# Performance work log

Hardware: AMD Instinct MI355X
Metric: run time of the kernel (lower is better)

Reference implementation:

```python
import jax, jax.numpy as jnp
import numpy as np

E, K = 8, 2              # n_routed_experts, num_experts_per_tok
H, I = 2048, 1408        # hidden_size, moe_intermediate_size
IS = 2 * I               # shared experts intermediate (n_shared_experts * I)
B, S = 2, 512


def setup_inputs() -> dict:
    key = jax.random.key(0)
    ks = jax.random.split(key, 8)
    w = 0.02
    return {
        "hidden_states": jax.random.normal(ks[0], (B, S, H), jnp.float32),
        "router_w": jax.random.normal(ks[1], (E, H), jnp.float32) * w,
        "w_gate": jax.random.normal(ks[2], (E, I, H), jnp.float32) * w,
        "w_up": jax.random.normal(ks[3], (E, I, H), jnp.float32) * w,
        "w_down": jax.random.normal(ks[4], (E, H, I), jnp.float32) * w,
        "sw_gate": jax.random.normal(ks[5], (IS, H), jnp.float32) * w,
        "sw_up": jax.random.normal(ks[6], (IS, H), jnp.float32) * w,
        "sw_down": jax.random.normal(ks[7], (H, IS), jnp.float32) * w,
    }


def reference(hidden_states, router_w, w_gate, w_up, w_down, sw_gate, sw_up, sw_down):
    b, s, h = hidden_states.shape
    x = hidden_states.reshape(-1, h)                      # [T, H]
    t = x.shape[0]

    # Router: F.linear(x, gate_weight) -> softmax (fp32) -> topk (sorted)
    router_logits = x @ router_w.T                        # [T, E]
    scores = jax.nn.softmax(router_logits.astype(jnp.float32), axis=-1)
    routing_weights, selected = jax.lax.top_k(scores, K)  # [T, K]
    routing_weights = routing_weights / (routing_weights.sum(-1, keepdims=True) + 1e-6)
    routing_weights = routing_weights.astype(x.dtype)

    # Combine weights: [T, E], zero where expert not selected (exact gather/scatter math)
    cw = jnp.zeros((t, E), x.dtype).at[jnp.arange(t)[:, None], selected].add(routing_weights)

    # Per-expert SwiGLU FFN, batched over experts (grouped GEMM form)
    g = jnp.einsum('td,eid->eti', x, w_gate)              # [E, T, I]
    u = jnp.einsum('td,eid->eti', x, w_up)                # [E, T, I]
    y = jnp.einsum('eti,edi->etd', jax.nn.silu(g) * u, w_down)  # [E, T, H]
    moe_out = jnp.einsum('etd,te->td', y, cw)             # weighted combine -> [T, H]

    # Shared experts SwiGLU over all tokens
    shared = (jax.nn.silu(x @ sw_gate.T) * (x @ sw_up.T)) @ sw_down.T  # [T, H]

    final = (moe_out + shared).reshape(b, s, h)
    return final, router_logits
```

## Files before the change

kernel.cpp:

```cpp
#include <hip/hip_runtime.h>
#include <hip/hip_bf16.h>
#include <math.h>

#define T_TOK 1024
#define HDIM  2048
#define NEXP  8
#define IDIM  1408
#define ISH   2816
#define ROW_CAP 3072
#define ROWS_ALL 4096
#define MOE_TILES 24
#define NT_TOT 32

typedef __attribute__((ext_vector_type(8))) short bf16x8;
typedef __attribute__((ext_vector_type(4))) float f32x4;

static __device__ __forceinline__ unsigned short f2bf(float f) {
  __hip_bfloat16 h = __float2bfloat16(f);
  return __builtin_bit_cast(unsigned short, h);
}

__global__ __launch_bounds__(256) void router_kernel(
    const float* __restrict__ x, const float* __restrict__ rw,
    float* __restrict__ logits_out, int* __restrict__ selk, float* __restrict__ cwk)
{
  int t = blockIdx.x;
  int tid = threadIdx.x;
  float part[NEXP];
  const float* xr = x + (size_t)t * HDIM + tid * 8;
  float4 xa = *reinterpret_cast<const float4*>(xr);
  float4 xb = *reinterpret_cast<const float4*>(xr + 4);
  for (int e = 0; e < NEXP; ++e) {
    const float* wp = rw + (size_t)e * HDIM + tid * 8;
    float4 wa = *reinterpret_cast<const float4*>(wp);
    float4 wb = *reinterpret_cast<const float4*>(wp + 4);
    part[e] = xa.x*wa.x + xa.y*wa.y + xa.z*wa.z + xa.w*wa.w
            + xb.x*wb.x + xb.y*wb.y + xb.z*wb.z + xb.w*wb.w;
  }
  for (int e = 0; e < NEXP; ++e)
    for (int off = 32; off; off >>= 1)
      part[e] += __shfl_xor(part[e], off, 64);
  __shared__ float sums[4][NEXP];
  int wid = tid >> 6, lane = tid & 63;
  if (lane == 0) for (int e = 0; e < NEXP; ++e) sums[wid][e] = part[e];
  __syncthreads();
  if (tid == 0) {
    float lg[NEXP];
    for (int e = 0; e < NEXP; ++e) lg[e] = sums[0][e] + sums[1][e] + sums[2][e] + sums[3][e];
    float mx = lg[0];
    for (int e = 1; e < NEXP; ++e) mx = fmaxf(mx, lg[e]);
    float p[NEXP], s = 0.f;
    for (int e = 0; e < NEXP; ++e) { p[e] = expf(lg[e] - mx); s += p[e]; }
    for (int e = 0; e < NEXP; ++e) p[e] /= s;
    int i1 = 0;
    for (int e = 1; e < NEXP; ++e) if (lg[e] > lg[i1]) i1 = e;
    int i2 = -1;
    for (int e = 0; e < NEXP; ++e) { if (e == i1) continue; if (i2 < 0 || lg[e] > lg[i2]) i2 = e; }
    float denom = p[i1] + p[i2] + 1e-6f;
    selk[t*2] = i1; selk[t*2+1] = i2;
    cwk[t*2] = p[i1] / denom; cwk[t*2+1] = p[i2] / denom;
    for (int e = 0; e < NEXP; ++e) logits_out[t * NEXP + e] = lg[e];
  }
}

__global__ __launch_bounds__(512) void plan_kernel(
    const int* __restrict__ selk, const float* __restrict__ cwk,
    int* __restrict__ rowidx, int* __restrict__ tok_of_row,
    float* __restrict__ rowwgt, int* __restrict__ tile_tab)
{
  __shared__ int cnt[NEXP];
  __shared__ int seg[NEXP];
  int tid = threadIdx.x;
  int w = tid >> 6, lane = tid & 63;
  for (int i = tid; i < ROW_CAP; i += 512) { tok_of_row[i] = -1; rowwgt[i] = 0.f; }
  for (int i = tid; i < T_TOK; i += 512) { tok_of_row[ROW_CAP + i] = i; rowwgt[ROW_CAP + i] = 1.f; }
  int total = 0;
  for (int base = 0; base < 2 * T_TOK; base += 64) {
    unsigned long long m = __ballot(selk[base + lane] == w);
    total += __popcll(m);
  }
  if (lane == 0) cnt[w] = total;
  __syncthreads();
  if (tid == 0) {
    int s = 0;
    for (int e = 0; e < NEXP; ++e) { seg[e] = s; s += (cnt[e] + 127) & ~127; }
  }
  __syncthreads();
  int run = seg[w];
  for (int base = 0; base < 2 * T_TOK; base += 64) {
    int i = base + lane;
    bool f = selk[i] == w;
    unsigned long long m = __ballot(f);
    if (f) {
      int r = run + __popcll(m & ((1ull << lane) - 1ull));
      rowidx[i] = r;
      tok_of_row[r] = i >> 1;
      rowwgt[r] = cwk[i];
    }
    run += __popcll(m);
  }
  __syncthreads();
  if (tid < NT_TOT) {
    int e = -1, valid = 0;
    if (tid < MOE_TILES) {
      int base = tid * 128;
      for (int k = 0; k < NEXP; ++k) {
        int s0 = seg[k], s1 = s0 + ((cnt[k] + 127) & ~127);
        if (base >= s0 && base < s1) {
          e = k;
          valid = cnt[k] - (base - s0);
          if (valid > 128) valid = 128;
          if (valid < 0) valid = 0;
        }
      }
    } else { e = 0; valid = 128; }
    tile_tab[tid*2] = e;
    tile_tab[tid*2+1] = valid;
  }
}

__global__ __launch_bounds__(256) void gather_kernel(
    const float* __restrict__ x, const int* __restrict__ tok_of_row,
    unsigned short* __restrict__ xg)
{
  int r = blockIdx.x;
  int tid = threadIdx.x;
  int tok = tok_of_row[r];
  unsigned short* dst = xg + (size_t)r * HDIM + tid * 8;
  union { unsigned short us[8]; uint4 q; } p;
  if (tok < 0) {
    p.q = uint4{0, 0, 0, 0};
  } else {
    const float* src = x + (size_t)tok * HDIM + tid * 8;
    float4 a = *reinterpret_cast<const float4*>(src);
    float4 b = *reinterpret_cast<const float4*>(src + 4);
    p.us[0]=f2bf(a.x); p.us[1]=f2bf(a.y); p.us[2]=f2bf(a.z); p.us[3]=f2bf(a.w);
    p.us[4]=f2bf(b.x); p.us[5]=f2bf(b.y); p.us[6]=f2bf(b.z); p.us[7]=f2bf(b.w);
  }
  *reinterpret_cast<uint4*>(dst) = p.q;
}

static __device__ __forceinline__ void bwrite(
    unsigned short (*Bs)[72], int brow, int bc, const float4* v)
{
  union { unsigned short us[8]; uint4 q; } a, b;
  a.us[0]=f2bf(v[0].x); a.us[1]=f2bf(v[0].y); a.us[2]=f2bf(v[0].z); a.us[3]=f2bf(v[0].w);
  a.us[4]=f2bf(v[1].x); a.us[5]=f2bf(v[1].y); a.us[6]=f2bf(v[1].z); a.us[7]=f2bf(v[1].w);
  b.us[0]=f2bf(v[2].x); b.us[1]=f2bf(v[2].y); b.us[2]=f2bf(v[2].z); b.us[3]=f2bf(v[2].w);
  b.us[4]=f2bf(v[3].x); b.us[5]=f2bf(v[3].y); b.us[6]=f2bf(v[3].z); b.us[7]=f2bf(v[3].w);
  *reinterpret_cast<uint4*>(&Bs[brow][bc]) = a.q;
  *reinterpret_cast<uint4*>(&Bs[brow][bc + 8]) = b.q;
}

static __device__ __forceinline__ void bload(const float* __restrict__ src, float4* v)
{
  v[0] = *reinterpret_cast<const float4*>(src);
  v[1] = *reinterpret_cast<const float4*>(src + 4);
  v[2] = *reinterpret_cast<const float4*>(src + 8);
  v[3] = *reinterpret_cast<const float4*>(src + 12);
}

static __device__ __forceinline__ void stage_a(
    const unsigned short* __restrict__ abase, size_t lda, int k0,
    unsigned short* As, int wid, int lane)
{
  #pragma unroll
  for (int j = 0; j < 2; ++j) {
    int row = j * 64 + wid * 8 + (lane >> 3);
    int col = ((lane & 7) ^ (row & 7)) << 3;
    const unsigned short* src = abase + (size_t)row * lda + k0 + col;
    unsigned short* dst = &As[(j * 64 + wid * 8) * 64];
    __builtin_amdgcn_global_load_lds(
        (const __attribute__((address_space(1))) void*)src,
        (__attribute__((address_space(3))) void*)dst, 16, 0, 0);
  }
}

__global__ __launch_bounds__(512) void gu_kernel(
    const unsigned short* __restrict__ xg,
    const float* __restrict__ w_gate, const float* __restrict__ w_up,
    const float* __restrict__ sw_gate, const float* __restrict__ sw_up,
    const float* __restrict__ rowwgt, const int* __restrict__ tile_tab,
    unsigned short* __restrict__ hg, unsigned short* __restrict__ hsh)
{
  int bid = blockIdx.x;
  int lb = (bid & 7) * 55 + (bid >> 3);
  int mt, nt;
  if (lb < MOE_TILES * 11) { mt = lb % MOE_TILES; nt = lb / MOE_TILES; }
  else { int s = lb - MOE_TILES * 11; mt = MOE_TILES + (s & 7); nt = s >> 3; }

  int e = tile_tab[mt*2], valid = tile_tab[mt*2+1];
  if (valid <= 0) return;
  bool sh = mt >= MOE_TILES;
  int m0 = mt * 128, n0 = nt * 128;
  const float *wg, *wu; unsigned short* hout; int ldo;
  if (sh) { wg = sw_gate; wu = sw_up; hout = hsh + (size_t)(m0 - ROW_CAP) * ISH; ldo = ISH; }
  else {
    size_t wo = (size_t)e * IDIM * HDIM;
    wg = w_gate + wo; wu = w_up + wo;
    hout = hg + (size_t)m0 * IDIM; ldo = IDIM;
  }

  __shared__ unsigned short As[128 * 64];
  __shared__ unsigned short BgS[128][72];
  __shared__ unsigned short BuS[128][72];

  int tid = threadIdx.x, wid = tid >> 6, lane = tid & 63;
  int wr = wid >> 2, wc = wid & 3;
  int fr = lane & 15, fq8 = (lane >> 4) << 3;

  f32x4 accg[4][2] = {{}};
  f32x4 accu[4][2] = {{}};

  int brow = tid >> 2, bc = (tid & 3) << 4;
  const float* gsrc = wg + (size_t)(n0 + brow) * HDIM + bc;
  const float* usrc = wu + (size_t)(n0 + brow) * HDIM + bc;
  const unsigned short* abase = xg + (size_t)m0 * HDIM;

  float4 pg[4], pu[4];
  bload(gsrc, pg); bload(usrc, pu);

  const int NK = HDIM / 64;
  for (int t = 0; t < NK; ++t) {
    int k1 = (t + 1 < NK) ? (t + 1) * 64 : 0;
    stage_a(abase, HDIM, t * 64, As, wid, lane);
    bwrite(BgS, brow, bc, pg);
    bwrite(BuS, brow, bc, pu);
    __syncthreads();
    bload(gsrc + k1, pg);
    bload(usrc + k1, pu);
    #pragma unroll
    for (int kk = 0; kk < 64; kk += 32) {
      bf16x8 a[4], bg[2], bu[2];
      #pragma unroll
      for (int m = 0; m < 4; ++m) {
        int row = wr * 64 + m * 16 + fr;
        a[m] = *reinterpret_cast<const bf16x8*>(&As[row * 64 + ((kk + fq8) ^ ((row & 7) << 3))]);
      }
      #pragma unroll
      for (int n = 0; n < 2; ++n) {
        bg[n] = *reinterpret_cast<const bf16x8*>(&BgS[wc * 32 + n * 16 + fr][kk + fq8]);
        bu[n] = *reinterpret_cast<const bf16x8*>(&BuS[wc * 32 + n * 16 + fr][kk + fq8]);
      }
      #pragma unroll
      for (int m = 0; m < 4; ++m)
        #pragma unroll
        for (int n = 0; n < 2; ++n) {
          accg[m][n] = __builtin_amdgcn_mfma_f32_16x16x32_bf16(a[m], bg[n], accg[m][n], 0, 0, 0);
          accu[m][n] = __builtin_amdgcn_mfma_f32_16x16x32_bf16(a[m], bu[n], accu[m][n], 0, 0, 0);
        }
    }
    __syncthreads();
  }

  int fq = lane >> 4;
  #pragma unroll
  for (int m = 0; m < 4; ++m)
    #pragma unroll
    for (int j = 0; j < 4; ++j) {
      int grow = wr * 64 + m * 16 + fq * 4 + j;
      float wv = rowwgt[m0 + grow];
      #pragma unroll
      for (int n = 0; n < 2; ++n) {
        float g = accg[m][n][j], u = accu[m][n][j];
        float hv = g / (1.f + __expf(-g)) * u * wv;
        hout[(size_t)grow * ldo + n0 + wc * 32 + n * 16 + fr] = f2bf(hv);
      }
    }
}

__global__ __launch_bounds__(512) void dn_kernel(
    const unsigned short* __restrict__ hg, const unsigned short* __restrict__ hsh,
    const float* __restrict__ w_down, const float* __restrict__ sw_down,
    const int* __restrict__ tile_tab,
    float* __restrict__ ydn, float* __restrict__ outf)
{
  int bid = blockIdx.x;
  int lb = (bid & 7) * 64 + (bid >> 3);
  int mt, nt;
  if (lb < MOE_TILES * 16) { mt = lb % MOE_TILES; nt = lb / MOE_TILES; }
  else { int s = lb - MOE_TILES * 16; mt = MOE_TILES + (s & 7); nt = s >> 3; }

  int e = tile_tab[mt*2], valid = tile_tab[mt*2+1];
  if (valid <= 0) return;
  bool sh = mt >= MOE_TILES;
  int m0 = mt * 128, n0 = nt * 128;
  const unsigned short* abase; const float* bbase; int K; float* obase;
  if (sh) { abase = hsh + (size_t)(m0 - ROW_CAP) * ISH; K = ISH; bbase = sw_down; obase = outf + (size_t)(m0 - ROW_CAP) * HDIM; }
  else { abase = hg + (size_t)m0 * IDIM; K = IDIM; bbase = w_down + (size_t)e * HDIM * IDIM; obase = ydn + (size_t)m0 * HDIM; }

  __shared__ unsigned short As[128 * 64];
  __shared__ unsigned short BsS[128][72];

  int tid = threadIdx.x, wid = tid >> 6, lane = tid & 63;
  int wr = wid >> 2, wc = wid & 3;
  int fr = lane & 15, fq8 = (lane >> 4) << 3;

  f32x4 acc[4][2] = {{}};

  int brow = tid >> 2, bc = (tid & 3) << 4;
  const float* bsrc = bbase + (size_t)(n0 + brow) * K + bc;

  float4 pb[4];
  bload(bsrc, pb);

  const int NK = K / 64;
  for (int t = 0; t < NK; ++t) {
    int k1 = (t + 1 < NK) ? (t + 1) * 64 : 0;
    stage_a(abase, K, t * 64, As, wid, lane);
    bwrite(BsS, brow, bc, pb);
    __syncthreads();
    bload(bsrc + k1, pb);
    #pragma unroll
    for (int kk = 0; kk < 64; kk += 32) {
      bf16x8 a[4], b[2];
      #pragma unroll
      for (int m = 0; m < 4; ++m) {
        int row = wr * 64 + m * 16 + fr;
        a[m] = *reinterpret_cast<const bf16x8*>(&As[row * 64 + ((kk + fq8) ^ ((row & 7) << 3))]);
      }
      #pragma unroll
      for (int n = 0; n < 2; ++n)
        b[n] = *reinterpret_cast<const bf16x8*>(&BsS[wc * 32 + n * 16 + fr][kk + fq8]);
      #pragma unroll
      for (int m = 0; m < 4; ++m)
        #pragma unroll
        for (int n = 0; n < 2; ++n)
          acc[m][n] = __builtin_amdgcn_mfma_f32_16x16x32_bf16(a[m], b[n], acc[m][n], 0, 0, 0);
    }
    __syncthreads();
  }
  int fq = lane >> 4;
  #pragma unroll
  for (int m = 0; m < 4; ++m)
    #pragma unroll
    for (int j = 0; j < 4; ++j) {
      int grow = wr * 64 + m * 16 + fq * 4 + j;
      #pragma unroll
      for (int n = 0; n < 2; ++n)
        obase[(size_t)grow * HDIM + n0 + wc * 32 + n * 16 + fr] = acc[m][n][j];
    }
}

__global__ __launch_bounds__(256) void combine_kernel(
    const float* __restrict__ ydn, const int* __restrict__ rowidx,
    float* __restrict__ outf)
{
  int t = blockIdx.x;
  int c = threadIdx.x * 8;
  int r0 = rowidx[t*2], r1 = rowidx[t*2+1];
  const float4* a0 = reinterpret_cast<const float4*>(ydn + (size_t)r0 * HDIM + c);
  const float4* a1 = reinterpret_cast<const float4*>(ydn + (size_t)r1 * HDIM + c);
  float4* o = reinterpret_cast<float4*>(outf + (size_t)t * HDIM + c);
  float4 x0 = a0[0], x1 = a0[1], y0 = a1[0], y1 = a1[1];
  float4 o0 = o[0], o1 = o[1];
  o0.x += x0.x + y0.x; o0.y += x0.y + y0.y; o0.z += x0.z + y0.z; o0.w += x0.w + y0.w;
  o1.x += x1.x + y1.x; o1.y += x1.y + y1.y; o1.z += x1.z + y1.z; o1.w += x1.w + y1.w;
  o[0] = o0; o[1] = o1;
}

extern "C" void kernel_launch(void* const* d_in, const int* in_sizes, int n_in,
                              void* d_out, int out_size, void* d_ws, size_t ws_size,
                              hipStream_t stream) {
  const float* x      = (const float*)d_in[0];
  const float* rw     = (const float*)d_in[1];
  const float* w_gate = (const float*)d_in[2];
  const float* w_up   = (const float*)d_in[3];
  const float* w_down = (const float*)d_in[4];
  const float* sw_g   = (const float*)d_in[5];
  const float* sw_u   = (const float*)d_in[6];
  const float* sw_d   = (const float*)d_in[7];
  float* out_final  = (float*)d_out;
  float* out_logits = out_final + (size_t)T_TOK * HDIM;

  char* ws = (char*)d_ws;
  int*   selk     = (int*)(ws + 0);
  float* cwk      = (float*)(ws + 8192);
  int*   rowidx   = (int*)(ws + 16384);
  int*   tokrow   = (int*)(ws + 24576);
  float* rowwgt   = (float*)(ws + 40960);
  int*   tile_tab = (int*)(ws + 57344);
  unsigned short* xg  = (unsigned short*)(ws + 65536);
  unsigned short* hg  = (unsigned short*)(ws + 65536 + 16777216);
  unsigned short* hsh = (unsigned short*)(ws + 65536 + 16777216 + 8650752);
  float* ydn = (float*)(ws + 65536 + 16777216 + 8650752 + 5767168);

  router_kernel<<<T_TOK, 256, 0, stream>>>(x, rw, out_logits, selk, cwk);
  plan_kernel<<<1, 512, 0, stream>>>(selk, cwk, rowidx, tokrow, rowwgt, tile_tab);
  gather_kernel<<<ROWS_ALL, 256, 0, stream>>>(x, tokrow, xg);
  gu_kernel<<<440, 512, 0, stream>>>(
      xg, w_gate, w_up, sw_g, sw_u, rowwgt, tile_tab, hg, hsh);
  dn_kernel<<<512, 512, 0, stream>>>(
      hg, hsh, w_down, sw_d, tile_tab, ydn, out_final);
  combine_kernel<<<T_TOK, 256, 0, stream>>>(ydn, rowidx, out_final);
}
```

Measured before the change: 311.8 us.

## Pre-convert expert weights to bf16 and stage B tiles via direct-to-LDS loads

Adds a weight-conversion kernel that turns the fp32 gate/up and down weights into bf16 workspace buffers before each GEMM stage. The GEMM kernels then load B tiles with global_load_lds into XOR-swizzled LDS, the same way A is loaded, replacing the register prefetch and in-kernel conversion. This cuts per-tile conversion work and register pressure, and halves the bytes each GEMM tile reads for weights. The cost is an extra full pass over all weights every call: an fp32 read plus a bf16 write and re-read. The register-level prefetch overlap of the B loads is also lost.

```diff
diff --git a/kernel.cpp b/kernel.cpp
--- a/kernel.cpp
+++ b/kernel.cpp
@@ -140,36 +140,38 @@
   *reinterpret_cast<uint4*>(dst) = p.q;
 }
 
-static __device__ __forceinline__ void bwrite(
-    unsigned short (*Bs)[72], int brow, int bc, const float4* v)
-{
-  union { unsigned short us[8]; uint4 q; } a, b;
-  a.us[0]=f2bf(v[0].x); a.us[1]=f2bf(v[0].y); a.us[2]=f2bf(v[0].z); a.us[3]=f2bf(v[0].w);
-  a.us[4]=f2bf(v[1].x); a.us[5]=f2bf(v[1].y); a.us[6]=f2bf(v[1].z); a.us[7]=f2bf(v[1].w);
-  b.us[0]=f2bf(v[2].x); b.us[1]=f2bf(v[2].y); b.us[2]=f2bf(v[2].z); b.us[3]=f2bf(v[2].w);
-  b.us[4]=f2bf(v[3].x); b.us[5]=f2bf(v[3].y); b.us[6]=f2bf(v[3].z); b.us[7]=f2bf(v[3].w);
-  *reinterpret_cast<uint4*>(&Bs[brow][bc]) = a.q;
-  *reinterpret_cast<uint4*>(&Bs[brow][bc + 8]) = b.q;
-}
-
-static __device__ __forceinline__ void bload(const float* __restrict__ src, float4* v)
-{
-  v[0] = *reinterpret_cast<const float4*>(src);
-  v[1] = *reinterpret_cast<const float4*>(src + 4);
-  v[2] = *reinterpret_cast<const float4*>(src + 8);
-  v[3] = *reinterpret_cast<const float4*>(src + 12);
-}
-
-static __device__ __forceinline__ void stage_a(
-    const unsigned short* __restrict__ abase, size_t lda, int k0,
-    unsigned short* As, int wid, int lane)
+__global__ __launch_bounds__(256) void wcvt_kernel(
+    const float* __restrict__ s0, const float* __restrict__ s1,
+    const float* __restrict__ s2, const float* __restrict__ s3,
+    unsigned short* __restrict__ d0, unsigned short* __restrict__ d1,
+    unsigned short* __restrict__ d2, unsigned short* __restrict__ d3,
+    int b0, int b1, int b2)
+{
+  int b = blockIdx.x;
+  const float* s; unsigned short* d; int off;
+  if (b < b0)      { s = s0; d = d0; off = b; }
+  else if (b < b1) { s = s1; d = d1; off = b - b0; }
+  else if (b < b2) { s = s2; d = d2; off = b - b1; }
+  else             { s = s3; d = d3; off = b - b2; }
+  size_t idx = (size_t)off * 2048 + threadIdx.x * 8;
+  float4 va = *reinterpret_cast<const float4*>(s + idx);
+  float4 vb = *reinterpret_cast<const float4*>(s + idx + 4);
+  union { unsigned short us[8]; uint4 q; } p;
+  p.us[0]=f2bf(va.x); p.us[1]=f2bf(va.y); p.us[2]=f2bf(va.z); p.us[3]=f2bf(va.w);
+  p.us[4]=f2bf(vb.x); p.us[5]=f2bf(vb.y); p.us[6]=f2bf(vb.z); p.us[7]=f2bf(vb.w);
+  *reinterpret_cast<uint4*>(d + idx) = p.q;
+}
+
+static __device__ __forceinline__ void stage_t(
+    const unsigned short* __restrict__ base, size_t ld, int k0,
+    unsigned short* Ls, int wid, int lane)
 {
   #pragma unroll
   for (int j = 0; j < 2; ++j) {
     int row = j * 64 + wid * 8 + (lane >> 3);
     int col = ((lane & 7) ^ (row & 7)) << 3;
-    const unsigned short* src = abase + (size_t)row * lda + k0 + col;
-    unsigned short* dst = &As[(j * 64 + wid * 8) * 64];
+    const unsigned short* src = base + (size_t)row * ld + k0 + col;
+    unsigned short* dst = &Ls[(j * 64 + wid * 8) * 64];
     __builtin_amdgcn_global_load_lds(
         (const __attribute__((address_space(1))) void*)src,
         (__attribute__((address_space(3))) void*)dst, 16, 0, 0);
@@ -178,8 +180,8 @@
 
 __global__ __launch_bounds__(512) void gu_kernel(
     const unsigned short* __restrict__ xg,
-    const float* __restrict__ w_gate, const float* __restrict__ w_up,
-    const float* __restrict__ sw_gate, const float* __restrict__ sw_up,
+    const unsigned short* __restrict__ wgb, const unsigned short* __restrict__ wub,
+    const unsigned short* __restrict__ swgb, const unsigned short* __restrict__ swub,
     const float* __restrict__ rowwgt, const int* __restrict__ tile_tab,
     unsigned short* __restrict__ hg, unsigned short* __restrict__ hsh)
 {
@@ -193,42 +195,34 @@
   if (valid <= 0) return;
   bool sh = mt >= MOE_TILES;
   int m0 = mt * 128, n0 = nt * 128;
-  const float *wg, *wu; unsigned short* hout; int ldo;
-  if (sh) { wg = sw_gate; wu = sw_up; hout = hsh + (size_t)(m0 - ROW_CAP) * ISH; ldo = ISH; }
+  const unsigned short *wg, *wu; unsigned short* hout; int ldo;
+  if (sh) { wg = swgb; wu = swub; hout = hsh + (size_t)(m0 - ROW_CAP) * ISH; ldo = ISH; }
   else {
     size_t wo = (size_t)e * IDIM * HDIM;
-    wg = w_gate + wo; wu = w_up + wo;
+    wg = wgb + wo; wu = wub + wo;
     hout = hg + (size_t)m0 * IDIM; ldo = IDIM;
   }
 
   __shared__ unsigned short As[128 * 64];
-  __shared__ unsigned short BgS[128][72];
-  __shared__ unsigned short BuS[128][72];
+  __shared__ unsigned short Bg[128 * 64];
+  __shared__ unsigned short Bu[128 * 64];
 
   int tid = threadIdx.x, wid = tid >> 6, lane = tid & 63;
   int wr = wid >> 2, wc = wid & 3;
-  int fr = lane & 15, fq8 = (lane >> 4) << 3;
+  int fr = lane & 15, fq = lane >> 4, fq8 = fq << 3;
 
   f32x4 accg[4][2] = {{}};
   f32x4 accu[4][2] = {{}};
 
-  int brow = tid >> 2, bc = (tid & 3) << 4;
-  const float* gsrc = wg + (size_t)(n0 + brow) * HDIM + bc;
-  const float* usrc = wu + (size_t)(n0 + brow) * HDIM + bc;
   const unsigned short* abase = xg + (size_t)m0 * HDIM;
-
-  float4 pg[4], pu[4];
-  bload(gsrc, pg); bload(usrc, pu);
-
-  const int NK = HDIM / 64;
-  for (int t = 0; t < NK; ++t) {
-    int k1 = (t + 1 < NK) ? (t + 1) * 64 : 0;
-    stage_a(abase, HDIM, t * 64, As, wid, lane);
-    bwrite(BgS, brow, bc, pg);
-    bwrite(BuS, brow, bc, pu);
+  const unsigned short* gb = wg + (size_t)n0 * HDIM;
+  const unsigned short* ub = wu + (size_t)n0 * HDIM;
+
+  for (int k0 = 0; k0 < HDIM; k0 += 64) {
+    stage_t(abase, HDIM, k0, As, wid, lane);
+    stage_t(gb,    HDIM, k0, Bg, wid, lane);
+    stage_t(ub,    HDIM, k0, Bu, wid, lane);
     __syncthreads();
-    bload(gsrc + k1, pg);
-    bload(usrc + k1, pu);
     #pragma unroll
     for (int kk = 0; kk < 64; kk += 32) {
       bf16x8 a[4], bg[2], bu[2];
@@ -239,8 +233,10 @@
       }
       #pragma unroll
       for (int n = 0; n < 2; ++n) {
-        bg[n] = *reinterpret_cast<const bf16x8*>(&BgS[wc * 32 + n * 16 + fr][kk + fq8]);
-        bu[n] = *reinterpret_cast<const bf16x8*>(&BuS[wc * 32 + n * 16 + fr][kk + fq8]);
+        int brow = wc * 32 + n * 16 + fr;
+        int boff = brow * 64 + ((kk + fq8) ^ ((brow & 7) << 3));
+        bg[n] = *reinterpret_cast<const bf16x8*>(&Bg[boff]);
+        bu[n] = *reinterpret_cast<const bf16x8*>(&Bu[boff]);
       }
       #pragma unroll
       for (int m = 0; m < 4; ++m)
@@ -253,7 +249,6 @@
     __syncthreads();
   }
 
-  int fq = lane >> 4;
   #pragma unroll
   for (int m = 0; m < 4; ++m)
     #pragma unroll
@@ -271,7 +266,7 @@
 
 __global__ __launch_bounds__(512) void dn_kernel(
     const unsigned short* __restrict__ hg, const unsigned short* __restrict__ hsh,
-    const float* __restrict__ w_down, const float* __restrict__ sw_down,
+    const unsigned short* __restrict__ wdb, const unsigned short* __restrict__ swdb,
     const int* __restrict__ tile_tab,
     float* __restrict__ ydn, float* __restrict__ outf)
 {
@@ -285,32 +280,25 @@
   if (valid <= 0) return;
   bool sh = mt >= MOE_TILES;
   int m0 = mt * 128, n0 = nt * 128;
-  const unsigned short* abase; const float* bbase; int K; float* obase;
-  if (sh) { abase = hsh + (size_t)(m0 - ROW_CAP) * ISH; K = ISH; bbase = sw_down; obase = outf + (size_t)(m0 - ROW_CAP) * HDIM; }
-  else { abase = hg + (size_t)m0 * IDIM; K = IDIM; bbase = w_down + (size_t)e * HDIM * IDIM; obase = ydn + (size_t)m0 * HDIM; }
+  const unsigned short* abase; const unsigned short* bbase; int K; float* obase;
+  if (sh) { abase = hsh + (size_t)(m0 - ROW_CAP) * ISH; K = ISH; bbase = swdb; obase = outf + (size_t)(m0 - ROW_CAP) * HDIM; }
+  else { abase = hg + (size_t)m0 * IDIM; K = IDIM; bbase = wdb + (size_t)e * HDIM * IDIM; obase = ydn + (size_t)m0 * HDIM; }
 
   __shared__ unsigned short As[128 * 64];
-  __shared__ unsigned short BsS[128][72];
+  __shared__ unsigned short Bs[128 * 64];
 
   int tid = threadIdx.x, wid = tid >> 6, lane = tid & 63;
   int wr = wid >> 2, wc = wid & 3;
-  int fr = lane & 15, fq8 = (lane >> 4) << 3;
+  int fr = lane & 15, fq = lane >> 4, fq8 = fq << 3;
 
   f32x4 acc[4][2] = {{}};
 
-  int brow = tid >> 2, bc = (tid & 3) << 4;
-  const float* bsrc = bbase + (size_t)(n0 + brow) * K + bc;
-
-  float4 pb[4];
-  bload(bsrc, pb);
-
-  const int NK = K / 64;
-  for (int t = 0; t < NK; ++t) {
-    int k1 = (t + 1 < NK) ? (t + 1) * 64 : 0;
-    stage_a(abase, K, t * 64, As, wid, lane);
-    bwrite(BsS, brow, bc, pb);
+  const unsigned short* bb = bbase + (size_t)n0 * K;
+
+  for (int k0 = 0; k0 < K; k0 += 64) {
+    stage_t(abase, K, k0, As, wid, lane);
+    stage_t(bb,    K, k0, Bs, wid, lane);
     __syncthreads();
-    bload(bsrc + k1, pb);
     #pragma unroll
     for (int kk = 0; kk < 64; kk += 32) {
       bf16x8 a[4], b[2];
@@ -320,8 +308,10 @@
         a[m] = *reinterpret_cast<const bf16x8*>(&As[row * 64 + ((kk + fq8) ^ ((row & 7) << 3))]);
       }
       #pragma unroll
-      for (int n = 0; n < 2; ++n)
-        b[n] = *reinterpret_cast<const bf16x8*>(&BsS[wc * 32 + n * 16 + fr][kk + fq8]);
+      for (int n = 0; n < 2; ++n) {
+        int brow = wc * 32 + n * 16 + fr;
+        b[n] = *reinterpret_cast<const bf16x8*>(&Bs[brow * 64 + ((kk + fq8) ^ ((brow & 7) << 3))]);
+      }
       #pragma unroll
       for (int m = 0; m < 4; ++m)
         #pragma unroll
@@ -330,7 +320,6 @@
     }
     __syncthreads();
   }
-  int fq = lane >> 4;
   #pragma unroll
   for (int m = 0; m < 4; ++m)
     #pragma unroll
@@ -380,17 +369,33 @@
   int*   tokrow   = (int*)(ws + 24576);
   float* rowwgt   = (float*)(ws + 40960);
   int*   tile_tab = (int*)(ws + 57344);
-  unsigned short* xg  = (unsigned short*)(ws + 65536);
-  unsigned short* hg  = (unsigned short*)(ws + 65536 + 16777216);
-  unsigned short* hsh = (unsigned short*)(ws + 65536 + 16777216 + 8650752);
-  float* ydn = (float*)(ws + 65536 + 16777216 + 8650752 + 5767168);
+  size_t off = 65536;
+  unsigned short* xg  = (unsigned short*)(ws + off);  off += (size_t)ROWS_ALL * HDIM * 2;
+  unsigned short* hg  = (unsigned short*)(ws + off);  off += (size_t)ROW_CAP * IDIM * 2;
+  unsigned short* hsh = (unsigned short*)(ws + off);  off += (size_t)T_TOK * ISH * 2;
+  float* ydn          = (float*)(ws + off);           off += (size_t)ROW_CAP * HDIM * 4;
+  unsigned short* wbuf = (unsigned short*)(ws + off);
+  unsigned short* wgb  = wbuf;
+  unsigned short* wub  = wgb + (size_t)NEXP * IDIM * HDIM;
+  unsigned short* swgb = wub + (size_t)NEXP * IDIM * HDIM;
+  unsigned short* swub = swgb + (size_t)ISH * HDIM;
+  unsigned short* wdb  = wbuf;
+  unsigned short* swdb = wdb + (size_t)NEXP * HDIM * IDIM;
 
   router_kernel<<<T_TOK, 256, 0, stream>>>(x, rw, out_logits, selk, cwk);
   plan_kernel<<<1, 512, 0, stream>>>(selk, cwk, rowidx, tokrow, rowwgt, tile_tab);
   gather_kernel<<<ROWS_ALL, 256, 0, stream>>>(x, tokrow, xg);
+
+  wcvt_kernel<<<28160, 256, 0, stream>>>(
+      w_gate, w_up, sw_g, sw_u, wgb, wub, swgb, swub, 11264, 22528, 25344);
+
   gu_kernel<<<440, 512, 0, stream>>>(
-      xg, w_gate, w_up, sw_g, sw_u, rowwgt, tile_tab, hg, hsh);
+      xg, wgb, wub, swgb, swub, rowwgt, tile_tab, hg, hsh);
+
+  wcvt_kernel<<<14080, 256, 0, stream>>>(
+      w_down, sw_d, sw_d, sw_d, wdb, swdb, swdb, swdb, 11264, 14080, 14080);
+
   dn_kernel<<<512, 512, 0, stream>>>(
-      hg, hsh, w_down, sw_d, tile_tab, ydn, out_final);
+      hg, hsh, wdb, swdb, tile_tab, ydn, out_final);
   combine_kernel<<<T_TOK, 256, 0, stream>>>(ydn, rowidx, out_final);
 }
```

Measured after the change: 288.2 us. 1.08x faster.
